# Kernel tuning notes

Hardware: AMD Instinct MI355X
Metric: run time of the kernel (lower is better)

## Reference

```python
import jax, jax.numpy as jnp
import numpy as np

DIM = 1024
NUM_HEADS = 16
HEAD_DIM = DIM // NUM_HEADS
GATE_HID = DIM // 4


def setup_inputs() -> dict:
    key = jax.random.key(0)
    ks = jax.random.split(key, 16)
    B, S, D = 2, 2048, DIM
    sc = 1.0 / np.sqrt(D)
    inp = {
        "h": jax.random.normal(ks[0], (B, S, D), jnp.float32),
        "x": jax.random.normal(ks[1], (B, S, D), jnp.float32),
        # attention projections, stored (in, out) so y = x @ W + b
        "Wq": jax.random.normal(ks[2], (D, D), jnp.float32) * sc,
        "bq": jnp.zeros((D,), jnp.float32),
        "Wk": jax.random.normal(ks[3], (D, D), jnp.float32) * sc,
        "bk": jnp.zeros((D,), jnp.float32),
        "Wv": jax.random.normal(ks[4], (D, D), jnp.float32) * sc,
        "bv": jnp.zeros((D,), jnp.float32),
        "Wo": jax.random.normal(ks[5], (D, D), jnp.float32) * sc,
        "bo": jnp.zeros((D,), jnp.float32),
        # gating MLP: Linear(2D -> D//4) -> GELU -> Linear(D//4 -> D) -> sigmoid
        "Wg1": jax.random.normal(ks[6], (2 * D, GATE_HID), jnp.float32) * (1.0 / np.sqrt(2 * D)),
        "bg1": jnp.zeros((GATE_HID,), jnp.float32),
        "Wg2": jax.random.normal(ks[7], (GATE_HID, D), jnp.float32) * (1.0 / np.sqrt(GATE_HID)),
        "bg2": jnp.zeros((D,), jnp.float32),
    }
    return inp


def reference(h, x, Wq, bq, Wk, bk, Wv, bv, Wo, bo, Wg1, bg1, Wg2, bg2):
    B, S, D = h.shape
    # gated blend of latent h and input x
    gate_in = jnp.concatenate([h, x], axis=-1)                      # (B,S,2D)
    gate = jax.nn.sigmoid((jax.nn.gelu(gate_in @ Wg1 + bg1, approximate=False)) @ Wg2 + bg2)
    blended = gate * h + (1.0 - gate) * x                           # (B,S,D)
    # multi-head self-attention
    q = (blended @ Wq + bq).reshape(B, S, NUM_HEADS, HEAD_DIM)
    k = (blended @ Wk + bk).reshape(B, S, NUM_HEADS, HEAD_DIM)
    v = (blended @ Wv + bv).reshape(B, S, NUM_HEADS, HEAD_DIM)
    scale = 1.0 / np.sqrt(HEAD_DIM).astype(np.float32)
    scores = jnp.einsum('bqhd,bkhd->bhqk', q, k) * scale            # (B,H,S,S)
    attn = jax.nn.softmax(scores, axis=-1)
    out = jnp.einsum('bhqk,bkhd->bqhd', attn, v).reshape(B, S, D)
    return out @ Wo + bo
```

## Files before the change

kernel.cpp:

```cpp
#include <hip/hip_runtime.h>
#include <hip/hip_bf16.h>


typedef __attribute__((ext_vector_type(4))) unsigned int u32x4;
typedef __attribute__((ext_vector_type(2))) unsigned int u32x2;
typedef __attribute__((ext_vector_type(8))) short s16x8;
typedef __attribute__((ext_vector_type(8))) unsigned short u16x8;
typedef __attribute__((ext_vector_type(4))) float f32x4;

#define QSCALE 0.18033688011112043f
#define FIXED_M 24.0f

__device__ __forceinline__ unsigned short f2bf(float f) {
    unsigned int i = __builtin_bit_cast(unsigned int, f) + 0x8000u;
    return (unsigned short)(i >> 16);
}
__device__ __forceinline__ unsigned int pack2bf(float a, float b) {
    unsigned int ia = __builtin_bit_cast(unsigned int, a) + 0x8000u;
    unsigned int ib = __builtin_bit_cast(unsigned int, b) + 0x8000u;
    return __builtin_amdgcn_perm(ib, ia, 0x07060302u);
}

__device__ __forceinline__ void gload16(const void* g, void* l) {
    __builtin_amdgcn_global_load_lds(
        (const __attribute__((address_space(1))) void*)g,
        (__attribute__((address_space(3))) void*)l, 16, 0, 0);
}

struct TEntry { const float* src; unsigned short* dst; int K; int N; };
struct TTable { TEntry e[6]; };

__global__ __launch_bounds__(256) void prep_all(
    TTable tt,
    const float* __restrict__ bq, const float* __restrict__ bk,
    const float* __restrict__ bv, float* __restrict__ bqkv)
{
    const int bid = (int)blockIdx.x;
    const int tid = threadIdx.x;
    if (bid < 3072) {
        const TEntry E = tt.e[bid >> 9];
        const int bx = bid & 511;
        const int ntn = E.N >> 5;
        if (bx >= (E.K >> 6) * ntn) return;
        const int n0 = (bx % ntn) * 32, k0 = (bx / ntn) * 64;
        __shared__ float tile[64][33];
        const int lnn = tid & 31, lkk = tid >> 5;
#pragma unroll
        for (int i = 0; i < 8; ++i)
            tile[lkk + i * 8][lnn] = E.src[(size_t)(k0 + lkk + i * 8) * E.N + n0 + lnn];
        __syncthreads();
        const int snn = tid >> 3, skk = (tid & 7) * 8;
        u16x8 o;
#pragma unroll
        for (int j = 0; j < 8; ++j) o[j] = f2bf(tile[skk + j][snn]);
        *reinterpret_cast<u16x8*>(&E.dst[(size_t)(n0 + snn) * E.K + k0 + skk]) = o;
        return;
    }
    const int i = (bid - 3072) * 256 + tid;
    if (i < 1024) bqkv[i] = bq[i];
    else if (i < 2048) bqkv[i] = bk[i - 1024];
    else if (i < 3072) bqkv[i] = bv[i - 2048];
}

__global__ __launch_bounds__(256) void transpose_v(
    const unsigned short* __restrict__ qkv, unsigned short* __restrict__ vt)
{
    __shared__ unsigned short t[64][65];
    const int st = blockIdx.x;
    const int bh = blockIdx.y;
    const int b = bh >> 4, h = bh & 15;
    const int tx = threadIdx.x & 63, ty = threadIdx.x >> 6;
    const int s0 = st * 64;
    const size_t base = (size_t)(b * 2048 + s0) * 3072 + 2048 + h * 64;
#pragma unroll
    for (int i = 0; i < 16; ++i)
        t[ty + i * 4][tx] = qkv[base + (size_t)(ty + i * 4) * 3072 + tx];
    __syncthreads();
    const size_t obase = (size_t)(bh * 64) * 2048 + s0;
#pragma unroll
    for (int i = 0; i < 16; ++i)
        vt[obase + (size_t)(ty + i * 4) * 2048 + tx] = t[tx][ty + i * 4];
}

enum { EPI_GELU = 1, EPI_BLEND = 2, EPI_F32 = 3, EPI_QKV = 4 };

template <int EPI>
__global__ __launch_bounds__(256, 3) void gemm_kernel(
    const unsigned short* __restrict__ A, int lda,
    const unsigned short* __restrict__ Bt, int ldb,
    const float* __restrict__ bias,
    void* __restrict__ Cv, int ldc, int K,
    const float* __restrict__ hb, const float* __restrict__ xb,
    int swzn, int ntn)
{
    __shared__ unsigned short Alds[2][128 * 32];
    __shared__ unsigned short Blds[2][128 * 32];

    const int tid = threadIdx.x;
    const int lane = tid & 63;
    const int w = tid >> 6;
    const int wr = w >> 1, wc = w & 1;
    int mt, nt;
    if (swzn > 0) {
        const int xcd = (int)blockIdx.x & 7, seq = (int)blockIdx.x >> 3;
        nt = xcd * swzn + seq % swzn;
        mt = seq / swzn;
    } else {
        nt = (int)blockIdx.x % ntn;
        mt = (int)blockIdx.x / ntn;
    }
    const int m0 = mt * 128, n0 = nt * 128;
    const int lrow = lane & 15, lko = (lane >> 4) * 8;

    const int grow = w * 32 + (lane >> 2);
    const int gk8 = (lane & 3) * 8;
    const unsigned short* ga0 = A + (size_t)(m0 + grow) * lda + gk8;
    const unsigned short* ga1 = ga0 + (size_t)16 * lda;
    const unsigned short* gb0 = Bt + (size_t)(n0 + grow) * ldb + gk8;
    const unsigned short* gb1 = gb0 + (size_t)16 * ldb;

    auto stage = [&](int buf, int k0) {
        unsigned short* la = &Alds[buf][w * 1024];
        unsigned short* lb = &Blds[buf][w * 1024];
        gload16(ga0 + k0, la);
        gload16(ga1 + k0, la + 512);
        gload16(gb0 + k0, lb);
        gload16(gb1 + k0, lb + 512);
    };

    f32x4 acc[4][4];
#pragma unroll
    for (int i = 0; i < 4; ++i)
#pragma unroll
        for (int j = 0; j < 4; ++j) acc[i][j] = (f32x4){0.f, 0.f, 0.f, 0.f};

    const int kks = K >> 5;
    stage(0, 0);
    __syncthreads();

    for (int t = 0; t < kks; ++t) {
        const int cur = t & 1;
        if (t + 1 < kks) stage(cur ^ 1, (t + 1) << 5);

        s16x8 af[4], bfr[4];
#pragma unroll
        for (int mi = 0; mi < 4; ++mi)
            af[mi] = *reinterpret_cast<const s16x8*>(&Alds[cur][(wr * 64 + mi * 16 + lrow) * 32 + lko]);
#pragma unroll
        for (int ni = 0; ni < 4; ++ni)
            bfr[ni] = *reinterpret_cast<const s16x8*>(&Blds[cur][(wc * 64 + ni * 16 + lrow) * 32 + lko]);
#pragma unroll
        for (int mi = 0; mi < 4; ++mi)
#pragma unroll
            for (int ni = 0; ni < 4; ++ni)
                acc[mi][ni] = __builtin_amdgcn_mfma_f32_16x16x32_bf16(af[mi], bfr[ni], acc[mi][ni], 0, 0, 0);

        __syncthreads();
    }

    const int rbase = m0 + wr * 64;
    const int cbase = n0 + wc * 64;
#pragma unroll
    for (int mi = 0; mi < 4; ++mi) {
#pragma unroll
        for (int j = 0; j < 4; ++j) {
            const int r = rbase + mi * 16 + (lane >> 4) * 4 + j;
#pragma unroll
            for (int ni = 0; ni < 4; ++ni) {
                const int c = cbase + ni * 16 + (lane & 15);
                float v = acc[mi][ni][j] + bias[c];
                if constexpr (EPI == EPI_GELU) {
                    float g = 0.5f * v * (1.f + erff(v * 0.70710678118654752f));
                    ((unsigned short*)Cv)[(size_t)r * ldc + c] = f2bf(g);
                } else if constexpr (EPI == EPI_BLEND) {
                    float gate = 1.f / (1.f + __expf(-v));
                    const size_t o = (size_t)r * ldc + c;
                    float bl = gate * hb[o] + (1.f - gate) * xb[o];
                    ((unsigned short*)Cv)[o] = f2bf(bl);
                } else if constexpr (EPI == EPI_QKV) {
                    const float scl = (c < 1024) ? QSCALE : 1.f;
                    ((unsigned short*)Cv)[(size_t)r * ldc + c] = f2bf(v * scl);
                } else {
                    ((float*)Cv)[(size_t)r * ldc + c] = v;
                }
            }
        }
    }
}

template <int EPI>
__global__ __launch_bounds__(256, 4) void gemm64_kernel(
    const unsigned short* __restrict__ A, int lda,
    const unsigned short* __restrict__ Bt, int ldb,
    const float* __restrict__ bias,
    void* __restrict__ Cv, int ldc, int K,
    const float* __restrict__ hb, const float* __restrict__ xb,
    int swzn)
{
    __shared__ unsigned short Alds[2][64 * 32];
    __shared__ unsigned short Blds[2][64 * 32];

    const int tid = threadIdx.x;
    const int lane = tid & 63;
    const int w = tid >> 6;
    const int wr = w >> 1, wc = w & 1;
    const int xcd = (int)blockIdx.x & 7, seq = (int)blockIdx.x >> 3;
    const int nt = xcd * swzn + seq % swzn;
    const int mt = seq / swzn;
    const int m0 = mt * 64, n0 = nt * 64;
    const int lrow = lane & 15, lko = (lane >> 4) * 8;

    const int grow = w * 16 + (lane >> 2);
    const int gk8 = (lane & 3) * 8;
    const unsigned short* ga = A + (size_t)(m0 + grow) * lda + gk8;
    const unsigned short* gb = Bt + (size_t)(n0 + grow) * ldb + gk8;

    auto stage = [&](int buf, int k0) {
        gload16(ga + k0, &Alds[buf][w * 512]);
        gload16(gb + k0, &Blds[buf][w * 512]);
    };

    f32x4 acc[2][2];
#pragma unroll
    for (int i = 0; i < 2; ++i)
#pragma unroll
        for (int j = 0; j < 2; ++j) acc[i][j] = (f32x4){0.f, 0.f, 0.f, 0.f};

    const int kks = K >> 5;
    stage(0, 0);
    __syncthreads();

    for (int t = 0; t < kks; ++t) {
        const int cur = t & 1;
        if (t + 1 < kks) stage(cur ^ 1, (t + 1) << 5);

        s16x8 af[2], bfr[2];
#pragma unroll
        for (int mi = 0; mi < 2; ++mi)
            af[mi] = *reinterpret_cast<const s16x8*>(&Alds[cur][(wr * 32 + mi * 16 + lrow) * 32 + lko]);
#pragma unroll
        for (int ni = 0; ni < 2; ++ni)
            bfr[ni] = *reinterpret_cast<const s16x8*>(&Blds[cur][(wc * 32 + ni * 16 + lrow) * 32 + lko]);
#pragma unroll
        for (int mi = 0; mi < 2; ++mi)
#pragma unroll
            for (int ni = 0; ni < 2; ++ni)
                acc[mi][ni] = __builtin_amdgcn_mfma_f32_16x16x32_bf16(af[mi], bfr[ni], acc[mi][ni], 0, 0, 0);

        __syncthreads();
    }

    const int rbase = m0 + wr * 32;
    const int cbase = n0 + wc * 32;
#pragma unroll
    for (int mi = 0; mi < 2; ++mi) {
#pragma unroll
        for (int j = 0; j < 4; ++j) {
            const int r = rbase + mi * 16 + (lane >> 4) * 4 + j;
#pragma unroll
            for (int ni = 0; ni < 2; ++ni) {
                const int c = cbase + ni * 16 + (lane & 15);
                float v = acc[mi][ni][j] + bias[c];
                if constexpr (EPI == EPI_BLEND) {
                    float gate = 1.f / (1.f + __expf(-v));
                    const size_t o = (size_t)r * ldc + c;
                    float bl = gate * hb[o] + (1.f - gate) * xb[o];
                    ((unsigned short*)Cv)[o] = f2bf(bl);
                } else {
                    ((float*)Cv)[(size_t)r * ldc + c] = v;
                }
            }
        }
    }
}

__global__ __launch_bounds__(256, 2) void gemm_gelu64(
    const float* __restrict__ h, const float* __restrict__ x,
    const unsigned short* __restrict__ Bt, int ldb,
    const float* __restrict__ bias,
    unsigned short* __restrict__ C, int ldc, int K)
{
    __shared__ unsigned short Alds[2][64 * 32];
    __shared__ unsigned short Blds[2][64 * 32];

    const int tid = threadIdx.x;
    const int lane = tid & 63;
    const int w = tid >> 6;
    const int wr = w >> 1, wc = w & 1;
    const int nt = (int)blockIdx.x & 3, mt = (int)blockIdx.x >> 2;
    const int m0 = mt * 64, n0 = nt * 64;
    const int lrow = lane & 15, lko = (lane >> 4) * 8;

    const int grow = w * 16 + (lane >> 2);
    const int gk8 = (lane & 3) * 8;
    const unsigned short* gb = Bt + (size_t)(n0 + grow) * ldb + gk8;
    const size_t arow = (size_t)(m0 + grow) * 1024;

    auto loadA = [&](int k0, f32x4& lo, f32x4& hi) {
        const float* src = (k0 < 1024 ? h : x) + arow + (k0 & 1023) + gk8;
        lo = *reinterpret_cast<const f32x4*>(src);
        hi = *reinterpret_cast<const f32x4*>(src + 4);
    };
    auto writeA = [&](int buf, const f32x4& lo, const f32x4& hi) {
        u32x4 p = {pack2bf(lo[0], lo[1]), pack2bf(lo[2], lo[3]),
                   pack2bf(hi[0], hi[1]), pack2bf(hi[2], hi[3])};
        *reinterpret_cast<u32x4*>(&Alds[buf][grow * 32 + gk8]) = p;
    };

    f32x4 acc[2][2];
#pragma unroll
    for (int i = 0; i < 2; ++i)
#pragma unroll
        for (int j = 0; j < 2; ++j) acc[i][j] = (f32x4){0.f, 0.f, 0.f, 0.f};

    const int kks = K >> 5;
    f32x4 alo, ahi;
    loadA(0, alo, ahi);
    gload16(gb, &Blds[0][w * 512]);
    writeA(0, alo, ahi);
    __syncthreads();

    for (int t = 0; t < kks; ++t) {
        const int cur = t & 1;
        if (t + 1 < kks) {
            loadA((t + 1) << 5, alo, ahi);
            gload16(gb + ((t + 1) << 5), &Blds[cur ^ 1][w * 512]);
        }

        s16x8 af[2], bfr[2];
#pragma unroll
        for (int mi = 0; mi < 2; ++mi)
            af[mi] = *reinterpret_cast<const s16x8*>(&Alds[cur][(wr * 32 + mi * 16 + lrow) * 32 + lko]);
#pragma unroll
        for (int ni = 0; ni < 2; ++ni)
            bfr[ni] = *reinterpret_cast<const s16x8*>(&Blds[cur][(wc * 32 + ni * 16 + lrow) * 32 + lko]);
#pragma unroll
        for (int mi = 0; mi < 2; ++mi)
#pragma unroll
            for (int ni = 0; ni < 2; ++ni)
                acc[mi][ni] = __builtin_amdgcn_mfma_f32_16x16x32_bf16(af[mi], bfr[ni], acc[mi][ni], 0, 0, 0);

        if (t + 1 < kks) writeA(cur ^ 1, alo, ahi);
        __syncthreads();
    }

    const int rbase = m0 + wr * 32;
    const int cbase = n0 + wc * 32;
#pragma unroll
    for (int mi = 0; mi < 2; ++mi) {
#pragma unroll
        for (int j = 0; j < 4; ++j) {
            const int r = rbase + mi * 16 + (lane >> 4) * 4 + j;
#pragma unroll
            for (int ni = 0; ni < 2; ++ni) {
                const int c = cbase + ni * 16 + (lane & 15);
                float v = acc[mi][ni][j] + bias[c];
                float g = 0.5f * v * (1.f + erff(v * 0.70710678118654752f));
                C[(size_t)r * ldc + c] = f2bf(g);
            }
        }
    }
}

#define ALD 72

__global__ __launch_bounds__(256, 3) void attn_kernel(
    const unsigned short* __restrict__ qkv,
    const unsigned short* __restrict__ vt,
    unsigned short* __restrict__ out)
{
    __shared__ unsigned short Klds[2][64 * 64];
    __shared__ unsigned short Vlds[2][64 * 64];
    __shared__ unsigned short Plds[4][16 * ALD];

    const int tid = threadIdx.x, lane = tid & 63, w = tid >> 6;
    const int xcd = (int)blockIdx.x & 7, seq = (int)blockIdx.x >> 3;
    const int bh = xcd * 4 + (seq & 3);
    const int qt = seq >> 2;
    const int b = bh >> 4, h = bh & 15;
    const int rb = b * 2048;
    const int lrow = lane & 15, g = lane >> 4, lko = g * 8;

    s16x8 qf[2][2];
#pragma unroll
    for (int qg = 0; qg < 2; ++qg) {
        const size_t qrow = (size_t)(rb + qt * 128 + w * 32 + qg * 16 + lrow) * 3072 + h * 64;
        qf[qg][0] = *reinterpret_cast<const s16x8*>(qkv + qrow + lko);
        qf[qg][1] = *reinterpret_cast<const s16x8*>(qkv + qrow + 32 + lko);
    }

    const int grow = w * 16 + (lane >> 3);
    const int gswz = ((lane & 7) ^ (lane >> 3)) * 8;
    const unsigned short* kgp = qkv + (size_t)(rb + grow) * 3072 + 1024 + h * 64 + gswz;
    const unsigned short* vgp = vt + (size_t)(bh * 64 + grow) * 2048 + gswz;

    auto stage = [&](int buf, int t0) {
        gload16(kgp + (size_t)t0 * 3072, &Klds[buf][w * 1024]);
        gload16(kgp + (size_t)(t0 + 8) * 3072, &Klds[buf][w * 1024 + 512]);
        gload16(vgp + t0, &Vlds[buf][w * 1024]);
        gload16(vgp + t0 + 8 * 2048, &Vlds[buf][w * 1024 + 512]);
    };

    const int cs0 = ((g) ^ (lrow & 7)) * 8;
    const int cs1 = ((4 + g) ^ (lrow & 7)) * 8;

    f32x4 acc0[4], acc1[4];
#pragma unroll
    for (int di = 0; di < 4; ++di) {
        acc0[di] = (f32x4){0.f, 0.f, 0.f, 0.f};
        acc1[di] = (f32x4){0.f, 0.f, 0.f, 0.f};
    }
    float lsum0 = 0.f, lsum1 = 0.f;

    unsigned short* pw = &Plds[w][0];
    s16x8 vf[2][4];

    stage(0, 0);
    __syncthreads();

    for (int t0 = 0; t0 < 2048; t0 += 64) {
        const int cur = (t0 >> 6) & 1;
        if (t0 + 64 < 2048) stage(cur ^ 1, t0 + 64);

        if (t0 > 0) {
#pragma unroll
            for (int st = 0; st < 2; ++st) {
                s16x8 pf = *reinterpret_cast<const s16x8*>(&pw[lrow * ALD + st * 32 + lko]);
#pragma unroll
                for (int di = 0; di < 4; ++di)
                    acc1[di] = __builtin_amdgcn_mfma_f32_16x16x32_bf16(vf[st][di], pf, acc1[di], 0, 0, 0);
            }
        }

        s16x8 kf[4][2];
#pragma unroll
        for (int ni = 0; ni < 4; ++ni) {
            kf[ni][0] = *reinterpret_cast<const s16x8*>(&Klds[cur][(ni * 16 + lrow) * 64 + cs0]);
            kf[ni][1] = *reinterpret_cast<const s16x8*>(&Klds[cur][(ni * 16 + lrow) * 64 + cs1]);
        }

        f32x4 s0[4];
#pragma unroll
        for (int ni = 0; ni < 4; ++ni) s0[ni] = (f32x4){0.f, 0.f, 0.f, 0.f};
#pragma unroll
        for (int ni = 0; ni < 4; ++ni)
#pragma unroll
            for (int fi = 0; fi < 2; ++fi)
                s0[ni] = __builtin_amdgcn_mfma_f32_16x16x32_bf16(kf[ni][fi], qf[0][fi], s0[ni], 0, 0, 0);

#pragma unroll
        for (int ni = 0; ni < 4; ++ni) {
            float p0 = __builtin_amdgcn_exp2f(s0[ni][0] - FIXED_M);
            float p1 = __builtin_amdgcn_exp2f(s0[ni][1] - FIXED_M);
            float p2 = __builtin_amdgcn_exp2f(s0[ni][2] - FIXED_M);
            float p3 = __builtin_amdgcn_exp2f(s0[ni][3] - FIXED_M);
            lsum0 += (p0 + p1) + (p2 + p3);
            u32x2 pk = {pack2bf(p0, p1), pack2bf(p2, p3)};
            *reinterpret_cast<u32x2*>(&pw[lrow * ALD + ni * 16 + g * 4]) = pk;
        }

        f32x4 s1[4];
#pragma unroll
        for (int ni = 0; ni < 4; ++ni) s1[ni] = (f32x4){0.f, 0.f, 0.f, 0.f};
#pragma unroll
        for (int ni = 0; ni < 4; ++ni)
#pragma unroll
            for (int fi = 0; fi < 2; ++fi)
                s1[ni] = __builtin_amdgcn_mfma_f32_16x16x32_bf16(kf[ni][fi], qf[1][fi], s1[ni], 0, 0, 0);

#pragma unroll
        for (int di = 0; di < 4; ++di) {
            vf[0][di] = *reinterpret_cast<const s16x8*>(&Vlds[cur][(di * 16 + lrow) * 64 + cs0]);
            vf[1][di] = *reinterpret_cast<const s16x8*>(&Vlds[cur][(di * 16 + lrow) * 64 + cs1]);
        }

#pragma unroll
        for (int st = 0; st < 2; ++st) {
            s16x8 pf = *reinterpret_cast<const s16x8*>(&pw[lrow * ALD + st * 32 + lko]);
#pragma unroll
            for (int di = 0; di < 4; ++di)
                acc0[di] = __builtin_amdgcn_mfma_f32_16x16x32_bf16(vf[st][di], pf, acc0[di], 0, 0, 0);
        }

#pragma unroll
        for (int ni = 0; ni < 4; ++ni) {
            float p0 = __builtin_amdgcn_exp2f(s1[ni][0] - FIXED_M);
            float p1 = __builtin_amdgcn_exp2f(s1[ni][1] - FIXED_M);
            float p2 = __builtin_amdgcn_exp2f(s1[ni][2] - FIXED_M);
            float p3 = __builtin_amdgcn_exp2f(s1[ni][3] - FIXED_M);
            lsum1 += (p0 + p1) + (p2 + p3);
            u32x2 pk = {pack2bf(p0, p1), pack2bf(p2, p3)};
            *reinterpret_cast<u32x2*>(&pw[lrow * ALD + ni * 16 + g * 4]) = pk;
        }

        __syncthreads();
    }

#pragma unroll
    for (int st = 0; st < 2; ++st) {
        s16x8 pf = *reinterpret_cast<const s16x8*>(&pw[lrow * ALD + st * 32 + lko]);
#pragma unroll
        for (int di = 0; di < 4; ++di)
            acc1[di] = __builtin_amdgcn_mfma_f32_16x16x32_bf16(vf[st][di], pf, acc1[di], 0, 0, 0);
    }

    lsum0 += __shfl_xor(lsum0, 16);
    lsum0 += __shfl_xor(lsum0, 32);
    lsum1 += __shfl_xor(lsum1, 16);
    lsum1 += __shfl_xor(lsum1, 32);
    const float inv0 = 1.f / lsum0;
    const float inv1 = 1.f / lsum1;
    const size_t orow0 = (size_t)(rb + qt * 128 + w * 32 + lrow) * 1024 + h * 64;
    const size_t orow1 = orow0 + (size_t)16 * 1024;
#pragma unroll
    for (int di = 0; di < 4; ++di) {
        u32x2 ov0 = {pack2bf(acc0[di][0] * inv0, acc0[di][1] * inv0),
                     pack2bf(acc0[di][2] * inv0, acc0[di][3] * inv0)};
        *reinterpret_cast<u32x2*>(&out[orow0 + di * 16 + g * 4]) = ov0;
        u32x2 ov1 = {pack2bf(acc1[di][0] * inv1, acc1[di][1] * inv1),
                     pack2bf(acc1[di][2] * inv1, acc1[di][3] * inv1)};
        *reinterpret_cast<u32x2*>(&out[orow1 + di * 16 + g * 4]) = ov1;
    }
}

extern "C" void kernel_launch(void* const* d_in, const int* in_sizes, int n_in,
                              void* d_out, int out_size, void* d_ws, size_t ws_size,
                              hipStream_t stream)
{
    const float* h   = (const float*)d_in[0];
    const float* x   = (const float*)d_in[1];
    const float* Wq  = (const float*)d_in[2];
    const float* bq  = (const float*)d_in[3];
    const float* Wk  = (const float*)d_in[4];
    const float* bk  = (const float*)d_in[5];
    const float* Wv  = (const float*)d_in[6];
    const float* bv  = (const float*)d_in[7];
    const float* Wo  = (const float*)d_in[8];
    const float* bo  = (const float*)d_in[9];
    const float* Wg1 = (const float*)d_in[10];
    const float* bg1 = (const float*)d_in[11];
    const float* Wg2 = (const float*)d_in[12];
    const float* bg2 = (const float*)d_in[13];

    char* ws = (char*)d_ws;
    size_t off = 0;
    auto alloc = [&](size_t bytes) {
        void* p = ws + off;
        off += (bytes + 255) & ~(size_t)255;
        return p;
    };
    unsigned short* wg1T  = (unsigned short*)alloc((size_t)256 * 2048 * 2);
    unsigned short* wg2T  = (unsigned short*)alloc((size_t)1024 * 256 * 2);
    unsigned short* wqkvT = (unsigned short*)alloc((size_t)3072 * 1024 * 2);
    unsigned short* woT   = (unsigned short*)alloc((size_t)1024 * 1024 * 2);
    float*          bqkv  = (float*)alloc((size_t)3072 * 4);
    unsigned short* blend = (unsigned short*)alloc((size_t)4096 * 1024 * 2);
    unsigned short* attno = (unsigned short*)alloc((size_t)4096 * 1024 * 2);
    unsigned short* vtb   = (unsigned short*)alloc((size_t)32 * 64 * 2048 * 2);
    unsigned short* g1    = (unsigned short*)alloc((size_t)4096 * 256 * 2);
    unsigned short* qkv   = (unsigned short*)alloc((size_t)4096 * 3072 * 2);
    (void)ws_size; (void)in_sizes; (void)n_in; (void)out_size;

    TTable tt;
    tt.e[0] = {Wg1, wg1T, 2048, 256};
    tt.e[1] = {Wg2, wg2T, 256, 1024};
    tt.e[2] = {Wq, wqkvT, 1024, 1024};
    tt.e[3] = {Wk, wqkvT + (size_t)1024 * 1024, 1024, 1024};
    tt.e[4] = {Wv, wqkvT + (size_t)2048 * 1024, 1024, 1024};
    tt.e[5] = {Wo, woT, 1024, 1024};
    prep_all<<<3072 + 12, 256, 0, stream>>>(tt, bq, bk, bv, bqkv);

    gemm_gelu64<<<256, 256, 0, stream>>>(h, x, wg1T, 2048, bg1, g1, 256, 2048);
    gemm64_kernel<EPI_BLEND><<<1024, 256, 0, stream>>>(
        g1, 256, wg2T, 256, bg2, blend, 1024, 256, h, x, 2);

    gemm_kernel<EPI_QKV><<<768, 256, 0, stream>>>(
        blend, 1024, wqkvT, 1024, bqkv, qkv, 3072, 1024, nullptr, nullptr, 3, 24);

    transpose_v<<<dim3(32, 32), 256, 0, stream>>>(qkv, vtb);

    attn_kernel<<<512, 256, 0, stream>>>(qkv, vtb, attno);

    gemm64_kernel<EPI_F32><<<1024, 256, 0, stream>>>(
        attno, 1024, woT, 1024, bo, (float*)d_out, 1024, 1024, nullptr, nullptr, 2);
}
```

Baseline: 164.9 us.

## Split-K the gate GEMM1 into partial sums plus a GELU reduce kernel

Replaces the single 256-block gate GEMM (K=2048) with a 4-way split-K kernel of 512 blocks, each covering 32 rows by all 256 columns over a 512-wide K slice and writing fp32 partials into the qkv scratch buffer. A new reduce kernel sums the four partials, adds the bias, applies exact GELU and stores bf16. The aim is more parallelism and fewer redundant reads of the A operand across column tiles on a machine with many CUs. The cost is an extra launch and about 16 MB of fp32 partial traffic to and from memory.

```diff
diff --git a/kernel.cpp b/kernel.cpp
--- a/kernel.cpp
+++ b/kernel.cpp
@@ -6,6 +6,7 @@
 typedef __attribute__((ext_vector_type(2))) unsigned int u32x2;
 typedef __attribute__((ext_vector_type(8))) short s16x8;
 typedef __attribute__((ext_vector_type(8))) unsigned short u16x8;
+typedef __attribute__((ext_vector_type(4))) unsigned short u16x4;
 typedef __attribute__((ext_vector_type(4))) float f32x4;
 
 #define QSCALE 0.18033688011112043f
@@ -274,92 +275,111 @@
     }
 }
 
-__global__ __launch_bounds__(256, 2) void gemm_gelu64(
+__global__ __launch_bounds__(256, 4) void gelu_partial(
     const float* __restrict__ h, const float* __restrict__ x,
-    const unsigned short* __restrict__ Bt, int ldb,
-    const float* __restrict__ bias,
-    unsigned short* __restrict__ C, int ldc, int K)
-{
-    __shared__ unsigned short Alds[2][64 * 32];
-    __shared__ unsigned short Blds[2][64 * 32];
+    const unsigned short* __restrict__ Bt,
+    float* __restrict__ partial)
+{
+    __shared__ unsigned short Alds[2][32 * 32];
+    __shared__ unsigned short Blds[2][256 * 32];
 
     const int tid = threadIdx.x;
     const int lane = tid & 63;
     const int w = tid >> 6;
-    const int wr = w >> 1, wc = w & 1;
-    const int nt = (int)blockIdx.x & 3, mt = (int)blockIdx.x >> 2;
-    const int m0 = mt * 64, n0 = nt * 64;
+    const int mt = (int)blockIdx.x >> 2, ks = (int)blockIdx.x & 3;
+    const int m0 = mt * 32, kbase = ks * 512;
     const int lrow = lane & 15, lko = (lane >> 4) * 8;
 
-    const int grow = w * 16 + (lane >> 2);
-    const int gk8 = (lane & 3) * 8;
-    const unsigned short* gb = Bt + (size_t)(n0 + grow) * ldb + gk8;
-    const size_t arow = (size_t)(m0 + grow) * 1024;
-
-    auto loadA = [&](int k0, f32x4& lo, f32x4& hi) {
-        const float* src = (k0 < 1024 ? h : x) + arow + (k0 & 1023) + gk8;
-        lo = *reinterpret_cast<const f32x4*>(src);
-        hi = *reinterpret_cast<const f32x4*>(src + 4);
+    const int arl = tid >> 3, ac4 = (tid & 7) * 4;
+    const size_t arg = (size_t)(m0 + arl) * 1024;
+    auto loadA = [&](int k0, f32x4& v) {
+        v = *reinterpret_cast<const f32x4*>((k0 < 1024 ? h : x) + arg + (k0 & 1023) + ac4);
     };
-    auto writeA = [&](int buf, const f32x4& lo, const f32x4& hi) {
-        u32x4 p = {pack2bf(lo[0], lo[1]), pack2bf(lo[2], lo[3]),
-                   pack2bf(hi[0], hi[1]), pack2bf(hi[2], hi[3])};
-        *reinterpret_cast<u32x4*>(&Alds[buf][grow * 32 + gk8]) = p;
+    auto writeA = [&](int buf, const f32x4& v) {
+        u32x2 p = {pack2bf(v[0], v[1]), pack2bf(v[2], v[3])};
+        *reinterpret_cast<u32x2*>(&Alds[buf][arl * 32 + ac4]) = p;
     };
 
-    f32x4 acc[2][2];
+    const int brow = w * 64 + (lane >> 2);
+    const int bk8 = (lane & 3) * 8;
+    const unsigned short* gb = Bt + (size_t)brow * 2048 + kbase + bk8;
+    auto stageB = [&](int buf, int k0) {
+#pragma unroll
+        for (int i = 0; i < 4; ++i)
+            gload16(gb + (size_t)(i * 16) * 2048 + k0, &Blds[buf][(w * 64 + i * 16) * 32]);
+    };
+
+    f32x4 acc[2][4];
 #pragma unroll
     for (int i = 0; i < 2; ++i)
 #pragma unroll
-        for (int j = 0; j < 2; ++j) acc[i][j] = (f32x4){0.f, 0.f, 0.f, 0.f};
-
-    const int kks = K >> 5;
-    f32x4 alo, ahi;
-    loadA(0, alo, ahi);
-    gload16(gb, &Blds[0][w * 512]);
-    writeA(0, alo, ahi);
+        for (int j = 0; j < 4; ++j) acc[i][j] = (f32x4){0.f, 0.f, 0.f, 0.f};
+
+    f32x4 areg;
+    loadA(kbase, areg);
+    stageB(0, 0);
+    writeA(0, areg);
     __syncthreads();
 
-    for (int t = 0; t < kks; ++t) {
+    for (int t = 0; t < 16; ++t) {
         const int cur = t & 1;
-        if (t + 1 < kks) {
-            loadA((t + 1) << 5, alo, ahi);
-            gload16(gb + ((t + 1) << 5), &Blds[cur ^ 1][w * 512]);
-        }
-
-        s16x8 af[2], bfr[2];
+        if (t + 1 < 16) {
+            loadA(kbase + ((t + 1) << 5), areg);
+            stageB(cur ^ 1, (t + 1) << 5);
+        }
+
+        s16x8 af[2], bfr[4];
 #pragma unroll
         for (int mi = 0; mi < 2; ++mi)
-            af[mi] = *reinterpret_cast<const s16x8*>(&Alds[cur][(wr * 32 + mi * 16 + lrow) * 32 + lko]);
-#pragma unroll
-        for (int ni = 0; ni < 2; ++ni)
-            bfr[ni] = *reinterpret_cast<const s16x8*>(&Blds[cur][(wc * 32 + ni * 16 + lrow) * 32 + lko]);
+            af[mi] = *reinterpret_cast<const s16x8*>(&Alds[cur][(mi * 16 + lrow) * 32 + lko]);
+#pragma unroll
+        for (int ni = 0; ni < 4; ++ni)
+            bfr[ni] = *reinterpret_cast<const s16x8*>(&Blds[cur][(w * 64 + ni * 16 + lrow) * 32 + lko]);
 #pragma unroll
         for (int mi = 0; mi < 2; ++mi)
 #pragma unroll
-            for (int ni = 0; ni < 2; ++ni)
+            for (int ni = 0; ni < 4; ++ni)
                 acc[mi][ni] = __builtin_amdgcn_mfma_f32_16x16x32_bf16(af[mi], bfr[ni], acc[mi][ni], 0, 0, 0);
 
-        if (t + 1 < kks) writeA(cur ^ 1, alo, ahi);
+        if (t + 1 < 16) writeA(cur ^ 1, areg);
         __syncthreads();
     }
 
-    const int rbase = m0 + wr * 32;
-    const int cbase = n0 + wc * 32;
+    float* pbase = partial + (size_t)ks * 4096 * 256;
 #pragma unroll
     for (int mi = 0; mi < 2; ++mi) {
 #pragma unroll
         for (int j = 0; j < 4; ++j) {
-            const int r = rbase + mi * 16 + (lane >> 4) * 4 + j;
-#pragma unroll
-            for (int ni = 0; ni < 2; ++ni) {
-                const int c = cbase + ni * 16 + (lane & 15);
-                float v = acc[mi][ni][j] + bias[c];
-                float g = 0.5f * v * (1.f + erff(v * 0.70710678118654752f));
-                C[(size_t)r * ldc + c] = f2bf(g);
+            const int r = m0 + mi * 16 + (lane >> 4) * 4 + j;
+#pragma unroll
+            for (int ni = 0; ni < 4; ++ni) {
+                const int c = w * 64 + ni * 16 + (lane & 15);
+                pbase[(size_t)r * 256 + c] = acc[mi][ni][j];
             }
         }
     }
+}
+
+__global__ __launch_bounds__(256) void gelu_reduce(
+    const float* __restrict__ partial, const float* __restrict__ bias,
+    unsigned short* __restrict__ g1)
+{
+    const size_t idx = ((size_t)blockIdx.x * 256 + threadIdx.x) * 4;
+    const int c = (int)(idx & 255);
+    f32x4 s = *reinterpret_cast<const f32x4*>(partial + idx);
+#pragma unroll
+    for (int ks = 1; ks < 4; ++ks) {
+        f32x4 p = *reinterpret_cast<const f32x4*>(partial + (size_t)ks * 4096 * 256 + idx);
+        s[0] += p[0]; s[1] += p[1]; s[2] += p[2]; s[3] += p[3];
+    }
+    f32x4 bb = *reinterpret_cast<const f32x4*>(bias + c);
+    u16x4 o;
+#pragma unroll
+    for (int j = 0; j < 4; ++j) {
+        float v = s[j] + bb[j];
+        o[j] = f2bf(0.5f * v * (1.f + erff(v * 0.70710678118654752f)));
+    }
+    *reinterpret_cast<u16x4*>(g1 + idx) = o;
 }
 
 #define ALD 72
@@ -559,6 +579,7 @@
     unsigned short* vtb   = (unsigned short*)alloc((size_t)32 * 64 * 2048 * 2);
     unsigned short* g1    = (unsigned short*)alloc((size_t)4096 * 256 * 2);
     unsigned short* qkv   = (unsigned short*)alloc((size_t)4096 * 3072 * 2);
+    float* partial = (float*)qkv;
     (void)ws_size; (void)in_sizes; (void)n_in; (void)out_size;
 
     TTable tt;
@@ -570,7 +591,8 @@
     tt.e[5] = {Wo, woT, 1024, 1024};
     prep_all<<<3072 + 12, 256, 0, stream>>>(tt, bq, bk, bv, bqkv);
 
-    gemm_gelu64<<<256, 256, 0, stream>>>(h, x, wg1T, 2048, bg1, g1, 256, 2048);
+    gelu_partial<<<512, 256, 0, stream>>>(h, x, wg1T, partial);
+    gelu_reduce<<<1024, 256, 0, stream>>>(partial, bg1, g1);
     gemm64_kernel<EPI_BLEND><<<1024, 256, 0, stream>>>(
         g1, 256, wg2T, 256, bg2, blend, 1024, 256, h, x, 2);
 
```

Measured after the change: 148.8 us. 9.8% less time.
